# Kernel tuning notes

Measured on AMD Instinct MI355X. Metric: run time of the kernel, lower is better.

Reference implementation:

```python
import jax, jax.numpy as jnp
from jax import lax
import numpy as np

# Heaviside spike with surrogate gradient (sdyt ~ d/dx tanh(x)); fwd is exact.
@jax.custom_vjp
def spike(x):
    return (x > 0).astype(x.dtype)

def _spike_fwd(x):
    return (x > 0).astype(x.dtype), x

def _spike_bwd(x, g):
    t = jnp.tanh(x)
    return (g * (1.0 - t * t),)

spike.defvjp(_spike_fwd, _spike_bwd)

def dyt(x, alpha, gamma, beta):
    # Dynamic Tanh norm: gamma * tanh(alpha * x) + beta
    return gamma * jnp.tanh(alpha * x) + beta

def slstm_seq(x, Wih, Whh, bih, bhh, thr, c0, h0):
    """Sequential SLSTM (snntorch, reset_mechanism='none') over a full sequence.
    x: [B,S,D]; Wih:[4H,D]; Whh:[4H,H]. Returns spikes [B,S,H], final (c, h)."""
    xg = jnp.einsum('bsd,gd->bsg', x, Wih) + bih  # precompute input gates [B,S,4H]

    def step(carry, xg_t):
        c, h = carry
        g = xg_t + h @ Whh.T + bhh
        i, f, gg, o = jnp.split(g, 4, axis=-1)  # torch LSTMCell gate order
        c = jax.nn.sigmoid(f) * c + jax.nn.sigmoid(i) * jnp.tanh(gg)
        h = jax.nn.sigmoid(o) * jnp.tanh(c)
        spk = spike(h - thr)
        return (c, h), spk

    (c, h), spks = lax.scan(step, (c0, h0), jnp.swapaxes(xg, 0, 1))
    return jnp.swapaxes(spks, 0, 1), c, h


def setup_inputs() -> dict:
    key = jax.random.key(0)
    ks = jax.random.split(key, 16)
    B, S, H, V, L = 4, 256, 512, 32000, 2
    G = 4 * H
    sc = 0.02
    d = {}
    d['src'] = jax.random.randint(ks[0], (B, S), 0, V)
    d['tgt'] = jax.random.randint(ks[1], (B, S), 0, V)
    d['emb_enc'] = jax.random.normal(ks[2], (V, H), jnp.float32) * sc
    d['enc_norm_alpha'] = jnp.full((1,), 0.5, jnp.float32)
    d['enc_norm_gamma'] = jnp.ones((H,), jnp.float32)
    d['enc_norm_beta'] = jnp.zeros((H,), jnp.float32)
    d['enc_Wih'] = jax.random.normal(ks[3], (L, G, H), jnp.float32) * sc
    d['enc_Whh'] = jax.random.normal(ks[4], (L, G, H), jnp.float32) * sc
    d['enc_bih'] = jnp.zeros((L, G), jnp.float32)
    d['enc_bhh'] = jnp.zeros((L, G), jnp.float32)
    d['enc_thr'] = jnp.ones((L, H), jnp.float32)
    d['emb_dec'] = jax.random.normal(ks[5], (V, H), jnp.float32) * sc
    d['dec_norm_alpha'] = jnp.full((1,), 0.5, jnp.float32)
    d['dec_norm_gamma'] = jnp.ones((H,), jnp.float32)
    d['dec_norm_beta'] = jnp.zeros((H,), jnp.float32)
    d['dec_Wih'] = jax.random.normal(ks[6], (L, G, H), jnp.float32) * sc
    d['dec_Whh'] = jax.random.normal(ks[7], (L, G, H), jnp.float32) * sc
    d['dec_bih'] = jnp.zeros((L, G), jnp.float32)
    d['dec_bhh'] = jnp.zeros((L, G), jnp.float32)
    d['dec_thr'] = jnp.ones((L, H), jnp.float32)
    d['dec_fc_W'] = jax.random.normal(ks[8], (L, H, H), jnp.float32) * sc
    d['dec_fc_b'] = jnp.zeros((L, H), jnp.float32)
    d['dec_dyt_alpha'] = jnp.full((L,), 0.5, jnp.float32)
    d['dec_dyt_gamma'] = jnp.ones((L, H), jnp.float32)
    d['dec_dyt_beta'] = jnp.zeros((L, H), jnp.float32)
    d['out_W'] = jax.random.normal(ks[9], (V, H), jnp.float32) * sc
    d['out_b'] = jnp.zeros((V,), jnp.float32)
    return d


def reference(src, tgt, emb_enc, enc_norm_alpha, enc_norm_gamma, enc_norm_beta,
              enc_Wih, enc_Whh, enc_bih, enc_bhh, enc_thr,
              emb_dec, dec_norm_alpha, dec_norm_gamma, dec_norm_beta,
              dec_Wih, dec_Whh, dec_bih, dec_bhh, dec_thr,
              dec_fc_W, dec_fc_b, dec_dyt_alpha, dec_dyt_gamma, dec_dyt_beta,
              out_W, out_b):
    L, _, H = enc_Wih.shape[0], enc_Wih.shape[1], enc_Wih.shape[2]
    B = src.shape[0]
    PAD = 0
    c0 = jnp.zeros((B, H), emb_enc.dtype)
    h0 = jnp.zeros((B, H), emb_enc.dtype)

    # ---- Encoder (note: non-bidirectional path feeds `src` to every layer, as in source) ----
    e_enc = emb_enc.at[PAD].set(0.0)  # padding_idx row is zero
    src_e = dyt(e_enc[src], enc_norm_alpha, enc_norm_gamma, enc_norm_beta)  # [B,S,H]
    syns, mems = [], []
    for l in range(L):
        _, c, h = slstm_seq(src_e, enc_Wih[l], enc_Whh[l], enc_bih[l], enc_bhh[l],
                            enc_thr[l], c0, h0)
        syns.append(c)
        mems.append(h)

    # ---- Decoder ----
    e_dec = emb_dec.at[PAD].set(0.0)
    x = dyt(e_dec[tgt], dec_norm_alpha, dec_norm_gamma, dec_norm_beta)  # [B,S,H]
    for l in range(L):
        spks, _, _ = slstm_seq(x, dec_Wih[l], dec_Whh[l], dec_bih[l], dec_bhh[l],
                               dec_thr[l], syns[l], mems[l])
        y = jnp.einsum('bsh,oh->bso', spks, dec_fc_W[l]) + dec_fc_b[l]
        if l > 0:  # residual=i>0
            y = y + x
        x = dyt(y, dec_dyt_alpha[l], dec_dyt_gamma[l], dec_dyt_beta[l])

    return jnp.einsum('bsh,vh->bsv', x, out_W) + out_b  # [B,S,V] logits
```

## Files before the change

### kernel.cpp

```cpp
#include <hip/hip_runtime.h>
#include <cstddef>

#define S_LEN 256
#define H_DIM 512

typedef __attribute__((ext_vector_type(8))) short bf16x8;
typedef __attribute__((ext_vector_type(4))) float f32x4;
typedef __attribute__((ext_vector_type(8))) unsigned short u16x8;

__device__ __forceinline__ float sigf(float x) { return 1.0f / (1.0f + expf(-x)); }

__device__ __forceinline__ unsigned short cvt_bf16(float f) {
  unsigned u = __float_as_uint(f);
  u += 0x7fffu + ((u >> 16) & 1u);
  return (unsigned short)(u >> 16);
}
__device__ __forceinline__ float bf2f(unsigned short s) {
  return __uint_as_float(((unsigned)s) << 16);
}

__global__ void zero_kernel(float* __restrict__ p, int n4) {
  int i = blockIdx.x * blockDim.x + threadIdx.x;
  if (i < n4) ((float4*)p)[i] = make_float4(0.f, 0.f, 0.f, 0.f);
}

__global__ __launch_bounds__(256)
void cvt_f32_bf16(const float* __restrict__ in, unsigned short* __restrict__ out,
                  int n4) {
  int i = blockIdx.x * blockDim.x + threadIdx.x;
  if (i < n4) {
    float4 v = ((const float4*)in)[i];
    ushort4 r;
    r.x = cvt_bf16(v.x); r.y = cvt_bf16(v.y);
    r.z = cvt_bf16(v.z); r.w = cvt_bf16(v.w);
    ((ushort4*)out)[i] = r;
  }
}

__global__ __launch_bounds__(128)
void embed_dyt(const int* __restrict__ idx, const float* __restrict__ E,
               const float* __restrict__ alpha_p, const float* __restrict__ gamma,
               const float* __restrict__ beta, unsigned short* __restrict__ out) {
  const int row = blockIdx.x;
  const int t4  = threadIdx.x * 4;
  const int id  = idx[row];
  const float al = alpha_p[0];
  float4 e = make_float4(0.f, 0.f, 0.f, 0.f);
  if (id != 0) e = *(const float4*)(E + (size_t)id * H_DIM + t4);
  const float4 g = *(const float4*)(gamma + t4);
  const float4 b = *(const float4*)(beta + t4);
  ushort4 o;
  o.x = cvt_bf16(g.x * tanhf(al * e.x) + b.x);
  o.y = cvt_bf16(g.y * tanhf(al * e.y) + b.y);
  o.z = cvt_bf16(g.z * tanhf(al * e.z) + b.z);
  o.w = cvt_bf16(g.w * tanhf(al * e.w) + b.w);
  *(ushort4*)(out + (size_t)row * H_DIM + t4) = o;
}

template<int ZSKIP>
__global__ __launch_bounds__(256)
void gemm_bt_bf16(const unsigned short* __restrict__ A,
                  const float* __restrict__ Bf,
                  const float* __restrict__ bias,
                  float* __restrict__ C, int N, int K) {
  __shared__ unsigned short As[128 * 64];
  __shared__ unsigned short Bs[128 * 64];
  __shared__ int nzf[4];
  const int tid = threadIdx.x;
  const int bm = blockIdx.x * 128, bn = blockIdx.y * 128;
  const int lane = tid & 63;
  const int wr = (tid >> 7) & 1, wc = (tid >> 6) & 1;
  f32x4 acc[4][4] = {};

  const int srow = tid >> 3;
  const int ss   = tid & 7;

  for (int k0 = 0; k0 < K; k0 += 64) {
    __syncthreads();
    if (ZSKIP) {
      unsigned nz = 0u;
#pragma unroll
      for (int p = 0; p < 4; ++p) {
        const int row = srow + p * 32;
        const int ps = ss ^ (row & 7);
        u16x8 va = *(const u16x8*)(A + (size_t)(bm + row) * K + k0 + ss * 8);
        *(u16x8*)(As + row * 64 + ps * 8) = va;
#pragma unroll
        for (int j = 0; j < 8; ++j) nz |= (unsigned)(unsigned short)va[j];
      }
      const int wnz = __any(nz != 0u) ? 1 : 0;
      if ((tid & 63) == 0) nzf[tid >> 6] = wnz;
      __syncthreads();
      if ((nzf[0] | nzf[1] | nzf[2] | nzf[3]) == 0) continue;
#pragma unroll
      for (int p = 0; p < 4; ++p) {
        const int row = srow + p * 32;
        const int ps = ss ^ (row & 7);
        const float* bp = Bf + (size_t)(bn + row) * K + k0 + ss * 8;
        const float4 b0 = *(const float4*)(bp);
        const float4 b1 = *(const float4*)(bp + 4);
        u16x8 vb;
        vb[0] = cvt_bf16(b0.x); vb[1] = cvt_bf16(b0.y);
        vb[2] = cvt_bf16(b0.z); vb[3] = cvt_bf16(b0.w);
        vb[4] = cvt_bf16(b1.x); vb[5] = cvt_bf16(b1.y);
        vb[6] = cvt_bf16(b1.z); vb[7] = cvt_bf16(b1.w);
        *(u16x8*)(Bs + row * 64 + ps * 8) = vb;
      }
      __syncthreads();
    } else {
#pragma unroll
      for (int p = 0; p < 4; ++p) {
        const int row = srow + p * 32;
        const int ps = ss ^ (row & 7);
        u16x8 va = *(const u16x8*)(A + (size_t)(bm + row) * K + k0 + ss * 8);
        *(u16x8*)(As + row * 64 + ps * 8) = va;
        const float* bp = Bf + (size_t)(bn + row) * K + k0 + ss * 8;
        const float4 b0 = *(const float4*)(bp);
        const float4 b1 = *(const float4*)(bp + 4);
        u16x8 vb;
        vb[0] = cvt_bf16(b0.x); vb[1] = cvt_bf16(b0.y);
        vb[2] = cvt_bf16(b0.z); vb[3] = cvt_bf16(b0.w);
        vb[4] = cvt_bf16(b1.x); vb[5] = cvt_bf16(b1.y);
        vb[6] = cvt_bf16(b1.z); vb[7] = cvt_bf16(b1.w);
        *(u16x8*)(Bs + row * 64 + ps * 8) = vb;
      }
      __syncthreads();
    }
#pragma unroll
    for (int ks = 0; ks < 2; ++ks) {
      const int r16 = lane & 15;
      const int kslot = ks * 4 + (lane >> 4);
      bf16x8 af[4], bfr[4];
#pragma unroll
      for (int m = 0; m < 4; ++m) {
        const int row = wr * 64 + m * 16 + r16;
        af[m] = *(const bf16x8*)(As + row * 64 + (kslot ^ (row & 7)) * 8);
      }
#pragma unroll
      for (int n = 0; n < 4; ++n) {
        const int row = wc * 64 + n * 16 + r16;
        bfr[n] = *(const bf16x8*)(Bs + row * 64 + (kslot ^ (row & 7)) * 8);
      }
#pragma unroll
      for (int m = 0; m < 4; ++m)
#pragma unroll
        for (int n = 0; n < 4; ++n)
          acc[m][n] = __builtin_amdgcn_mfma_f32_16x16x32_bf16(af[m], bfr[n],
                                                              acc[m][n], 0, 0, 0);
    }
  }

  const int r16 = lane & 15, rg = lane >> 4;
#pragma unroll
  for (int m = 0; m < 4; ++m) {
#pragma unroll
    for (int n = 0; n < 4; ++n) {
      const int col = bn + wc * 64 + n * 16 + r16;
      const float bb = bias[col];
      const int rowb = bm + wr * 64 + m * 16 + rg * 4;
#pragma unroll
      for (int r = 0; r < 4; ++r)
        C[(size_t)(rowb + r) * N + col] = acc[m][n][r] + bb;
    }
  }
}

__device__ __forceinline__ void rec_core(
    int g, int t, int tid,
    const float* __restrict__ xg, int xg_stride,
    const unsigned short* __restrict__ Whh, const float* __restrict__ bhh,
    const float* __restrict__ h_in, float* __restrict__ h_out,
    float* __restrict__ c,
    float* __restrict__ spk, const float* __restrict__ thr,
    float* __restrict__ hs, float (*__restrict__ gred)[4]) {
  const int lr = tid >> 3, kc = tid & 7;
  const int q = lr >> 3, ci = lr & 7;
  const int c0 = g * 8;
  const int grow = q * H_DIM + c0 + ci;
  float xgv[4] = {0.f, 0.f, 0.f, 0.f};
  if (kc == 0) {
#pragma unroll
    for (int b = 0; b < 4; ++b)
      xgv[b] = xg[(size_t)(b * S_LEN + t) * xg_stride + grow];
  }
  {
    const float4* s4 = (const float4*)h_in;
    float4* d4 = (float4*)hs;
    d4[tid] = s4[tid];
    d4[tid + 256] = s4[tid + 256];
  }
  __syncthreads();
  const unsigned short* wrow = Whh + (size_t)grow * H_DIM;
  float acc[4] = {0.f, 0.f, 0.f, 0.f};
#pragma unroll
  for (int it = 0; it < 8; ++it) {
    const int k = it * 64 + kc * 8;
    const u16x8 wv = *(const u16x8*)(wrow + k);
    const float w0 = bf2f(wv[0]), w1 = bf2f(wv[1]), w2 = bf2f(wv[2]), w3 = bf2f(wv[3]);
    const float w4 = bf2f(wv[4]), w5 = bf2f(wv[5]), w6 = bf2f(wv[6]), w7 = bf2f(wv[7]);
#pragma unroll
    for (int b = 0; b < 4; ++b) {
      const float4 hA = *(const float4*)&hs[b * H_DIM + k];
      const float4 hB = *(const float4*)&hs[b * H_DIM + k + 4];
      acc[b] += w0 * hA.x + w1 * hA.y + w2 * hA.z + w3 * hA.w
              + w4 * hB.x + w5 * hB.y + w6 * hB.z + w7 * hB.w;
    }
  }
#pragma unroll
  for (int off = 1; off < 8; off <<= 1) {
#pragma unroll
    for (int b = 0; b < 4; ++b) acc[b] += __shfl_xor(acc[b], off);
  }
  if (kc == 0) {
    const float bb = bhh[grow];
#pragma unroll
    for (int b = 0; b < 4; ++b) gred[lr][b] = acc[b] + xgv[b] + bb;
  }
  __syncthreads();
  if (tid < 32) {
    const int b = tid & 3, cc = tid >> 2;
    const int col = c0 + cc;
    const float gi = gred[cc][b];
    const float gf = gred[8 + cc][b];
    const float gg = gred[16 + cc][b];
    const float go = gred[24 + cc][b];
    const float cold = c[b * H_DIM + col];
    const float cn = sigf(gf) * cold + sigf(gi) * tanhf(gg);
    const float hn = sigf(go) * tanhf(cn);
    c[b * H_DIM + col] = cn;
    h_out[b * H_DIM + col] = hn;
    if (spk)
      spk[(size_t)(b * S_LEN + t) * H_DIM + col] = (hn - thr[col]) > 0.f ? 1.f : 0.f;
  }
}

struct StepInst {
  const float* xg;
  const unsigned short* Whh;
  const float* bhh;
  float* c;
  const float* h_in;
  float* h_out;
  int xg_stride;
};

__global__ __launch_bounds__(256)
void slstm_step(StepInst I0, StepInst I1, int t) {
  __shared__ float hs[4 * H_DIM];
  __shared__ float gred[32][4];
  StepInst I = (blockIdx.x < 64) ? I0 : I1;
  rec_core(blockIdx.x & 63, t, threadIdx.x, I.xg, I.xg_stride, I.Whh, I.bhh,
           I.h_in, I.h_out, I.c, nullptr, nullptr, hs, gred);
}

struct DecArgs {
  const float* xg0;
  float*       xg1;
  const unsigned short* Whh0bf; const unsigned short* Whh1bf;
  const float* bhh0; const float* bhh1;
  const unsigned short* Wih1bf; const float* bih1;
  const float* fc0W; const float* fc0b;
  const float* fc1W; const float* fc1b;
  const float* dyt_a;
  const float* dyt_g;
  const float* dyt_b;
  const float* thr0; const float* thr1;
  float* c0; float* c1;
  const float* h0_init; const float* h1_init;
  float* ring0; float* ring1;
  float* spk0; float* spk1;
  float* x1;
  unsigned short* x2;
};

__device__ __forceinline__ void stage_rows(const float* __restrict__ src, int t,
                                           int tid, float* dst) {
  float4* d4 = (float4*)dst;
  const int f0 = tid, f1 = tid + 256;
  d4[f0] = *(const float4*)(src + (size_t)((f0 >> 7) * S_LEN + t) * H_DIM + (f0 & 127) * 4);
  d4[f1] = *(const float4*)(src + (size_t)((f1 >> 7) * S_LEN + t) * H_DIM + (f1 & 127) * 4);
}

__global__ __launch_bounds__(256)
void dec_slot(DecArgs A, int s) {
  __shared__ float hs[4 * H_DIM];
  __shared__ float gred[32][4];
  const int bid = blockIdx.x;
  const int tid = threadIdx.x;

  if (bid < 64) {
    const int t = s;
    if (t < 256) {
      const float* h_in = (t == 0) ? A.h0_init : (A.ring0 + (size_t)(t & 1) * 2048);
      float* h_out = A.ring0 + (size_t)((t + 1) & 1) * 2048;
      rec_core(bid, t, tid, A.xg0, 2048, A.Whh0bf, A.bhh0, h_in, h_out, A.c0,
               A.spk0, A.thr0, hs, gred);
    }
  } else if (bid < 128) {
    const int t = s - 3;
    if (t >= 0 && t < 256) {
      const float* h_in = (t == 0) ? A.h1_init : (A.ring1 + (size_t)(t & 1) * 2048);
      float* h_out = A.ring1 + (size_t)((t + 1) & 1) * 2048;
      rec_core(bid - 64, t, tid, A.xg1, 2048, A.Whh1bf, A.bhh1, h_in, h_out, A.c1,
               A.spk1, A.thr1, hs, gred);
    }
  } else if (bid < 192) {
    const int t = s - 2;
    if (t >= 0 && t < 256) {
      stage_rows(A.x1, t, tid, hs);
      __syncthreads();
      const int wc = bid - 128;
      const int lr = tid >> 3, kc = tid & 7;
      const int row = wc * 32 + lr;
      const unsigned short* wrow = A.Wih1bf + (size_t)row * H_DIM;
      float acc[4] = {0.f, 0.f, 0.f, 0.f};
#pragma unroll
      for (int it = 0; it < 8; ++it) {
        const int k = it * 64 + kc * 8;
        const u16x8 wv = *(const u16x8*)(wrow + k);
        const float w0 = bf2f(wv[0]), w1 = bf2f(wv[1]), w2 = bf2f(wv[2]), w3 = bf2f(wv[3]);
        const float w4 = bf2f(wv[4]), w5 = bf2f(wv[5]), w6 = bf2f(wv[6]), w7 = bf2f(wv[7]);
#pragma unroll
        for (int b = 0; b < 4; ++b) {
          const float4 hA = *(const float4*)&hs[b * H_DIM + k];
          const float4 hB = *(const float4*)&hs[b * H_DIM + k + 4];
          acc[b] += w0 * hA.x + w1 * hA.y + w2 * hA.z + w3 * hA.w
                  + w4 * hB.x + w5 * hB.y + w6 * hB.z + w7 * hB.w;
        }
      }
#pragma unroll
      for (int off = 1; off < 8; off <<= 1) {
#pragma unroll
        for (int b = 0; b < 4; ++b) acc[b] += __shfl_xor(acc[b], off);
      }
      if (kc == 0) {
        const float bb = A.bih1[row];
#pragma unroll
        for (int b = 0; b < 4; ++b)
          A.xg1[(size_t)(b * S_LEN + t) * 2048 + row] = acc[b] + bb;
      }
    }
  } else {
    const bool isB = (bid < 224);
    const int t = isB ? (s - 1) : (s - 4);
    if (t >= 0 && t < 256) {
      const float* spk = isB ? A.spk0 : A.spk1;
      const float* fcW = isB ? A.fc0W : A.fc1W;
      const float* fcb = isB ? A.fc0b : A.fc1b;
      const int lidx = isB ? 0 : 1;
      stage_rows(spk, t, tid, hs);
      __syncthreads();
      const int wb = bid - (isB ? 192 : 224);
      const int lr = tid >> 4, kc = tid & 15;
      const int col = wb * 16 + lr;
      const float* wrow = fcW + (size_t)col * H_DIM;
      float a0 = 0.f, a1 = 0.f, a2 = 0.f, a3 = 0.f;
#pragma unroll
      for (int it = 0; it < 8; ++it) {
        const int k = kc * 32 + it * 4;
        const float4 w  = *(const float4*)(wrow + k);
        const float4 h0 = *(const float4*)&hs[0 * H_DIM + k];
        const float4 h1 = *(const float4*)&hs[1 * H_DIM + k];
        const float4 h2 = *(const float4*)&hs[2 * H_DIM + k];
        const float4 h3 = *(const float4*)&hs[3 * H_DIM + k];
        a0 += w.x * h0.x + w.y * h0.y + w.z * h0.z + w.w * h0.w;
        a1 += w.x * h1.x + w.y * h1.y + w.z * h1.z + w.w * h1.w;
        a2 += w.x * h2.x + w.y * h2.y + w.z * h2.z + w.w * h2.w;
        a3 += w.x * h3.x + w.y * h3.y + w.z * h3.z + w.w * h3.w;
      }
#pragma unroll
      for (int off = 1; off < 16; off <<= 1) {
        a0 += __shfl_xor(a0, off);
        a1 += __shfl_xor(a1, off);
        a2 += __shfl_xor(a2, off);
        a3 += __shfl_xor(a3, off);
      }
      if (kc == 0) {
        const float al = A.dyt_a[lidx];
        const float gm = A.dyt_g[lidx * H_DIM + col];
        const float be = A.dyt_b[lidx * H_DIM + col];
        const float bb = fcb[col];
        float v[4] = {a0, a1, a2, a3};
#pragma unroll
        for (int b = 0; b < 4; ++b) {
          float y = v[b] + bb;
          if (!isB) y += A.x1[(size_t)(b * S_LEN + t) * H_DIM + col];
          const float r = gm * tanhf(al * y) + be;
          if (isB) A.x1[(size_t)(b * S_LEN + t) * H_DIM + col] = r;
          else     A.x2[(size_t)(b * S_LEN + t) * H_DIM + col] = cvt_bf16(r);
        }
      }
    }
  }
}

extern "C" void kernel_launch(void* const* d_in, const int* in_sizes, int n_in,
                              void* d_out, int out_size, void* d_ws, size_t ws_size,
                              hipStream_t stream) {
  (void)in_sizes; (void)n_in; (void)out_size; (void)ws_size;
  const int*   src       = (const int*)d_in[0];
  const int*   tgt       = (const int*)d_in[1];
  const float* emb_enc   = (const float*)d_in[2];
  const float* enc_alpha = (const float*)d_in[3];
  const float* enc_gamma = (const float*)d_in[4];
  const float* enc_beta  = (const float*)d_in[5];
  const float* enc_Wih   = (const float*)d_in[6];
  const float* enc_Whh   = (const float*)d_in[7];
  const float* enc_bih   = (const float*)d_in[8];
  const float* enc_bhh   = (const float*)d_in[9];
  const float* emb_dec   = (const float*)d_in[11];
  const float* dec_alpha = (const float*)d_in[12];
  const float* dec_gamma = (const float*)d_in[13];
  const float* dec_beta  = (const float*)d_in[14];
  const float* dec_Wih   = (const float*)d_in[15];
  const float* dec_Whh   = (const float*)d_in[16];
  const float* dec_bih   = (const float*)d_in[17];
  const float* dec_bhh   = (const float*)d_in[18];
  const float* dec_thr   = (const float*)d_in[19];
  const float* dec_fc_W  = (const float*)d_in[20];
  const float* dec_fc_b  = (const float*)d_in[21];
  const float* dyt_alpha = (const float*)d_in[22];
  const float* dyt_gamma = (const float*)d_in[23];
  const float* dyt_beta  = (const float*)d_in[24];
  const float* out_W     = (const float*)d_in[25];
  const float* out_b     = (const float*)d_in[26];
  float* out = (float*)d_out;

  float* ws = (float*)d_ws;
  float*          x1        = ws;
  float*          xg_enc    = ws + 524288;
  float*          xg_d0     = xg_enc;
  float*          xg_d1     = xg_enc + 2097152;
  float*          spk0      = ws + 4718592;
  float*          spk1      = ws + 5242880;
  unsigned short* src_e_bf  = (unsigned short*)(ws + 5767168);
  unsigned short* dec_x0_bf = (unsigned short*)(ws + 5898240);
  unsigned short* x2_bf     = (unsigned short*)(ws + 6029312);
  unsigned short* wbf       = (unsigned short*)(ws + 6160384);
  float* st = ws + 7660544;
  float* zbuf    = st;
  float* c0buf   = st + 2048;
  float* c1buf   = st + 4096;
  float* ring_e0 = st + 6144;
  float* ring_e1 = st + 10240;
  float* ring_d0 = st + 14336;
  float* ring_d1 = st + 18432;

  zero_kernel<<<6, 256, 0, stream>>>(st, 1536);
  embed_dyt<<<1024, 128, 0, stream>>>(src, emb_enc, enc_alpha, enc_gamma, enc_beta,
                                      src_e_bf);
  embed_dyt<<<1024, 128, 0, stream>>>(tgt, emb_dec, dec_alpha, dec_gamma, dec_beta,
                                      dec_x0_bf);

  cvt_f32_bf16<<<2048, 256, 0, stream>>>(enc_Whh, wbf, 524288);

  gemm_bt_bf16<0><<<dim3(8, 32), 256, 0, stream>>>(src_e_bf, enc_Wih, enc_bih,
                                                   xg_enc, 4096, 512);

  for (int t = 0; t < 256; ++t) {
    StepInst A, B;
    A.xg = xg_enc;        A.Whh = wbf;                A.bhh = enc_bhh;
    A.c = c0buf;
    A.h_in  = (t == 0) ? zbuf : ring_e0 + (t & 1) * 2048;
    A.h_out = ring_e0 + ((t + 1) & 1) * 2048;
    A.xg_stride = 4096;
    B.xg = xg_enc + 2048; B.Whh = wbf + 1048576;      B.bhh = enc_bhh + 2048;
    B.c = c1buf;
    B.h_in  = (t == 0) ? zbuf : ring_e1 + (t & 1) * 2048;
    B.h_out = ring_e1 + ((t + 1) & 1) * 2048;
    B.xg_stride = 4096;
    slstm_step<<<128, 256, 0, stream>>>(A, B, t);
  }

  cvt_f32_bf16<<<2048, 256, 0, stream>>>(dec_Whh, wbf, 524288);
  cvt_f32_bf16<<<1024, 256, 0, stream>>>(dec_Wih + 1048576, wbf + 2097152, 262144);

  gemm_bt_bf16<0><<<dim3(8, 16), 256, 0, stream>>>(dec_x0_bf, dec_Wih, dec_bih,
                                                   xg_d0, 2048, 512);

  DecArgs D;
  D.xg0 = xg_d0;              D.xg1 = xg_d1;
  D.Whh0bf = wbf;             D.Whh1bf = wbf + 1048576;
  D.bhh0 = dec_bhh;           D.bhh1 = dec_bhh + 2048;
  D.Wih1bf = wbf + 2097152;   D.bih1 = dec_bih + 2048;
  D.fc0W = dec_fc_W;          D.fc0b = dec_fc_b;
  D.fc1W = dec_fc_W + 262144; D.fc1b = dec_fc_b + 512;
  D.dyt_a = dyt_alpha;        D.dyt_g = dyt_gamma;     D.dyt_b = dyt_beta;
  D.thr0 = dec_thr;           D.thr1 = dec_thr + 512;
  D.c0 = c0buf;               D.c1 = c1buf;
  D.h0_init = ring_e0;        D.h1_init = ring_e1;
  D.ring0 = ring_d0;          D.ring1 = ring_d1;
  D.spk0 = spk0;              D.spk1 = spk1;
  D.x1 = x1;                  D.x2 = x2_bf;

  for (int s = 0; s < 260; ++s)
    dec_slot<<<256, 256, 0, stream>>>(D, s);

  gemm_bt_bf16<1><<<dim3(8, 250), 256, 0, stream>>>(x2_bf, out_W, out_b,
                                                    out, 32000, 512);
}
```

Before: 2.520 ms.

## Replace per-timestep encoder launches with persistent kernel using flag-based sync

```diff
diff --git a/kernel.cpp b/kernel.cpp
--- a/kernel.cpp
+++ b/kernel.cpp
@@ -165,6 +165,117 @@
   }
 }
 
+struct EncP {
+  const float* xg;
+  const unsigned short* Whh;
+  const float* bhh;
+  float* ring;
+  int* flags;
+  float* cfin;
+};
+
+__global__ __launch_bounds__(256)
+void enc_persist(EncP P0, EncP P1) {
+  const EncP P = (blockIdx.x < 64) ? P0 : P1;
+  const int g = blockIdx.x & 63;
+  const int tid = threadIdx.x;
+  __shared__ float hs[2048];
+  __shared__ float gred[32][4];
+  __shared__ float cst[32];
+  const int lr = tid >> 3, kc = tid & 7;
+  const int q = lr >> 3, ci = lr & 7;
+  const int c0 = g * 8;
+  const int grow = q * H_DIM + c0 + ci;
+  u16x8 w[8];
+  {
+    const unsigned short* wrow = P.Whh + (size_t)grow * H_DIM + kc * 8;
+#pragma unroll
+    for (int it = 0; it < 8; ++it) w[it] = *(const u16x8*)(wrow + it * 64);
+  }
+  const float bb = P.bhh[grow];
+  const float* xgp = P.xg + grow;
+  if (tid < 32) cst[tid] = 0.f;
+  int budget = 2000000;
+
+  for (int t = 0; t < 256; ++t) {
+    float xgv[4] = {0.f, 0.f, 0.f, 0.f};
+    if (kc == 0) {
+#pragma unroll
+      for (int b = 0; b < 4; ++b)
+        xgv[b] = xgp[(size_t)(b * S_LEN + t) * 4096];
+    }
+    if (t == 0) {
+#pragma unroll
+      for (int j = 0; j < 8; ++j) hs[j * 256 + tid] = 0.f;
+    } else {
+      if (tid < 64) {
+        const int* fp = P.flags + tid;
+        while (budget > 0) {
+          int v = __hip_atomic_load(fp, __ATOMIC_RELAXED, __HIP_MEMORY_SCOPE_AGENT);
+          if (v >= t) break;
+          __builtin_amdgcn_s_sleep(1);
+          --budget;
+        }
+      }
+      __syncthreads();
+      const float* slot = P.ring + (size_t)(t & 1) * 2048;
+#pragma unroll
+      for (int j = 0; j < 8; ++j)
+        hs[j * 256 + tid] = __hip_atomic_load(slot + j * 256 + tid,
+                                              __ATOMIC_RELAXED,
+                                              __HIP_MEMORY_SCOPE_AGENT);
+    }
+    __syncthreads();
+
+    float acc[4] = {0.f, 0.f, 0.f, 0.f};
+#pragma unroll
+    for (int it = 0; it < 8; ++it) {
+      const int k = it * 64 + kc * 8;
+      const u16x8 wv = w[it];
+      const float w0 = bf2f(wv[0]), w1 = bf2f(wv[1]), w2 = bf2f(wv[2]), w3 = bf2f(wv[3]);
+      const float w4 = bf2f(wv[4]), w5 = bf2f(wv[5]), w6 = bf2f(wv[6]), w7 = bf2f(wv[7]);
+#pragma unroll
+      for (int b = 0; b < 4; ++b) {
+        const float4 hA = *(const float4*)&hs[b * H_DIM + k];
+        const float4 hB = *(const float4*)&hs[b * H_DIM + k + 4];
+        acc[b] += w0 * hA.x + w1 * hA.y + w2 * hA.z + w3 * hA.w
+                + w4 * hB.x + w5 * hB.y + w6 * hB.z + w7 * hB.w;
+      }
+    }
+#pragma unroll
+    for (int off = 1; off < 8; off <<= 1) {
+#pragma unroll
+      for (int b = 0; b < 4; ++b) acc[b] += __shfl_xor(acc[b], off);
+    }
+    if (kc == 0) {
+#pragma unroll
+      for (int b = 0; b < 4; ++b) gred[lr][b] = acc[b] + xgv[b] + bb;
+    }
+    __syncthreads();
+
+    if (tid < 32) {
+      const int b = tid & 3, cc = tid >> 2;
+      const int col = c0 + cc;
+      const float gi = gred[cc][b];
+      const float gf = gred[8 + cc][b];
+      const float gg = gred[16 + cc][b];
+      const float go = gred[24 + cc][b];
+      const float cold = cst[tid];
+      const float cn = sigf(gf) * cold + sigf(gi) * tanhf(gg);
+      const float hn = sigf(go) * tanhf(cn);
+      cst[tid] = cn;
+      __hip_atomic_store(P.ring + (size_t)((t + 1) & 1) * 2048 + b * H_DIM + col,
+                         hn, __ATOMIC_RELAXED, __HIP_MEMORY_SCOPE_AGENT);
+      if (t == 255) P.cfin[b * H_DIM + col] = cn;
+    }
+    asm volatile("s_waitcnt vmcnt(0)" ::: "memory");
+    __syncthreads();
+    if (tid == 0)
+      __hip_atomic_store(P.flags + g, t + 1, __ATOMIC_RELAXED,
+                         __HIP_MEMORY_SCOPE_AGENT);
+  }
+}
+
 __device__ __forceinline__ void rec_core(
     int g, int t, int tid,
     const float* __restrict__ xg, int xg_stride,
@@ -232,25 +343,6 @@
     if (spk)
       spk[(size_t)(b * S_LEN + t) * H_DIM + col] = (hn - thr[col]) > 0.f ? 1.f : 0.f;
   }
-}
-
-struct StepInst {
-  const float* xg;
-  const unsigned short* Whh;
-  const float* bhh;
-  float* c;
-  const float* h_in;
-  float* h_out;
-  int xg_stride;
-};
-
-__global__ __launch_bounds__(256)
-void slstm_step(StepInst I0, StepInst I1, int t) {
-  __shared__ float hs[4 * H_DIM];
-  __shared__ float gred[32][4];
-  StepInst I = (blockIdx.x < 64) ? I0 : I1;
-  rec_core(blockIdx.x & 63, t, threadIdx.x, I.xg, I.xg_stride, I.Whh, I.bhh,
-           I.h_in, I.h_out, I.c, nullptr, nullptr, hs, gred);
 }
 
 struct DecArgs {
@@ -441,12 +533,14 @@
   float* zbuf    = st;
   float* c0buf   = st + 2048;
   float* c1buf   = st + 4096;
-  float* ring_e0 = st + 6144;
-  float* ring_e1 = st + 10240;
-  float* ring_d0 = st + 14336;
-  float* ring_d1 = st + 18432;
-
-  zero_kernel<<<6, 256, 0, stream>>>(st, 1536);
+  int*   iflags  = (int*)(st + 6144);
+  float* ring_e0 = st + 6272;
+  float* ring_e1 = st + 10368;
+  float* ring_d0 = st + 14464;
+  float* ring_d1 = st + 18560;
+
+  (void)zbuf;
+  zero_kernel<<<7, 256, 0, stream>>>(st, 1568);
   embed_dyt<<<1024, 128, 0, stream>>>(src, emb_enc, enc_alpha, enc_gamma, enc_beta,
                                       src_e_bf);
   embed_dyt<<<1024, 128, 0, stream>>>(tgt, emb_dec, dec_alpha, dec_gamma, dec_beta,
@@ -457,20 +551,12 @@
   gemm_bt_bf16<0><<<dim3(8, 32), 256, 0, stream>>>(src_e_bf, enc_Wih, enc_bih,
                                                    xg_enc, 4096, 512);
 
-  for (int t = 0; t < 256; ++t) {
-    StepInst A, B;
-    A.xg = xg_enc;        A.Whh = wbf;                A.bhh = enc_bhh;
-    A.c = c0buf;
-    A.h_in  = (t == 0) ? zbuf : ring_e0 + (t & 1) * 2048;
-    A.h_out = ring_e0 + ((t + 1) & 1) * 2048;
-    A.xg_stride = 4096;
-    B.xg = xg_enc + 2048; B.Whh = wbf + 1048576;      B.bhh = enc_bhh + 2048;
-    B.c = c1buf;
-    B.h_in  = (t == 0) ? zbuf : ring_e1 + (t & 1) * 2048;
-    B.h_out = ring_e1 + ((t + 1) & 1) * 2048;
-    B.xg_stride = 4096;
-    slstm_step<<<128, 256, 0, stream>>>(A, B, t);
-  }
+  EncP E0, E1;
+  E0.xg = xg_enc;        E0.Whh = wbf;            E0.bhh = enc_bhh;
+  E0.ring = ring_e0;     E0.flags = iflags;       E0.cfin = c0buf;
+  E1.xg = xg_enc + 2048; E1.Whh = wbf + 1048576;  E1.bhh = enc_bhh + 2048;
+  E1.ring = ring_e1;     E1.flags = iflags + 64;  E1.cfin = c1buf;
+  enc_persist<<<128, 256, 0, stream>>>(E0, E1);
 
   cvt_f32_bf16<<<2048, 256, 0, stream>>>(dec_Whh, wbf, 524288);
   cvt_f32_bf16<<<1024, 256, 0, stream>>>(dec_Wih + 1048576, wbf + 2097152, 262144);
```

Result: slower. 2.786 ms (+10.6%).
